# Optimization experiments

Measured on AMD Instinct MI355X. Metric: run time of the kernel, lower is better.

Reference implementation:

```python
import jax, jax.numpy as jnp
import numpy as np

B, S, T, C = 4, 2048, 2048, 256
TEMPERATURE = 0.1
CONF_THR = 0.2
NEG_INF = -jnp.inf


def setup_inputs() -> dict:
    key = jax.random.key(0)
    k1, k2, k3 = jax.random.split(key, 3)
    src_feats = jax.random.normal(k1, (B, S, C), dtype=jnp.float32)
    tgt_feats = jax.random.normal(k2, (B, T, C), dtype=jnp.float32)
    # variable valid lengths per batch (padding masks)
    src_lens = jnp.array([2048, 1800, 1500, 1024])
    tgt_lens = jnp.array([2048, 1600, 2000, 1200])
    src_mask = jnp.arange(S)[None, :] < src_lens[:, None]
    tgt_mask = jnp.arange(T)[None, :] < tgt_lens[:, None]
    W = jax.random.normal(k3, (C, C), dtype=jnp.float32) * (C ** -0.5)
    return {"src_feats": src_feats, "tgt_feats": tgt_feats,
            "src_mask": src_mask, "tgt_mask": tgt_mask, "W": W}


def reference(src_feats, tgt_feats, src_mask, tgt_mask, W):
    # NOTE: original module applies src_proj to BOTH src and tgt (tgt_proj unused)
    src = jnp.einsum('bsc,dc->bsd', src_feats, W)  # Linear, no bias
    tgt = jnp.einsum('btc,dc->btd', tgt_feats, W)
    scale = src.shape[-1] ** 0.5
    src = src / scale
    tgt = tgt / scale
    sim = jnp.einsum('bsc,btc->bst', src, tgt) / TEMPERATURE  # [B,S,T]
    sim1 = jnp.where(src_mask[:, :, None], sim, NEG_INF)
    sim2 = jnp.where(tgt_mask[:, None, :], sim, NEG_INF)
    conf_matrix = jax.nn.softmax(sim1, axis=1) * jax.nn.softmax(sim2, axis=2)
    # get_match (no_grad in original): mutual-max + threshold mask.
    # Returned as a dense boolean mask (jit-safe), instead of nonzero() indices.
    m = conf_matrix > CONF_THR
    m = m & (conf_matrix == jnp.max(conf_matrix, axis=2, keepdims=True)) \
          & (conf_matrix == jnp.max(conf_matrix, axis=1, keepdims=True))
    return conf_matrix, m
```

## Files before the change

### kernel.cpp

```cpp
#include <hip/hip_runtime.h>
#include <hip/hip_bf16.h>
#include <cstdint>
#include <cstddef>

#define B_ 4
#define S_ 2048
#define T_ 2048
#define C_ 256
#define K2_ 512
#define NEG_INF (-INFINITY)

typedef __attribute__((ext_vector_type(8)))  __bf16 bf16x8;
typedef __attribute__((ext_vector_type(16))) float  f32x16;

#define ROWPAT(r, lh) (((r) & 3) + 8 * ((r) >> 2) + 4 * (lh))

typedef __attribute__((address_space(3))) unsigned       as3_u32;
typedef __attribute__((address_space(1))) const unsigned as1_u32;

__device__ __forceinline__ void gload16(const void* g, void* l) {
    __builtin_amdgcn_global_load_lds((as1_u32*)g, (as3_u32*)l, 16, 0, 0);
}

__device__ __forceinline__ unsigned pack_hl(float v) {
    __bf16 h = (__bf16)v;
    __bf16 l = (__bf16)(v - (float)h);
    unsigned short hu = __builtin_bit_cast(unsigned short, h);
    unsigned short lu = __builtin_bit_cast(unsigned short, l);
    return (unsigned)hu | ((unsigned)lu << 16);
}

__global__ void build_masks_kernel(const void* __restrict__ src_mask,
                                   const void* __restrict__ tgt_mask,
                                   int* __restrict__ smask, int* __restrict__ tmask) {
    int i = blockIdx.x * blockDim.x + threadIdx.x;
    const unsigned char* sb = (const unsigned char*)src_mask;
    const unsigned char* tb = (const unsigned char*)tgt_mask;
    bool s_is_byte = (sb[1] != 0);
    bool t_is_byte = (tb[1] != 0);
    if (i < B_ * S_)
        smask[i] = s_is_byte ? (sb[i] != 0) : (((const int*)src_mask)[i] != 0);
    if (i < B_ * T_)
        tmask[i] = t_is_byte ? (tb[i] != 0) : (((const int*)tgt_mask)[i] != 0);
}

__global__ __launch_bounds__(256) void split_kernel(
    const float* __restrict__ in, unsigned* __restrict__ out, int n4)
{
    for (int i = blockIdx.x * blockDim.x + threadIdx.x; i < n4;
         i += gridDim.x * blockDim.x) {
        float4 x = ((const float4*)in)[i];
        uint4 o;
        o.x = pack_hl(x.x); o.y = pack_hl(x.y);
        o.z = pack_hl(x.z); o.w = pack_hl(x.w);
        ((uint4*)out)[i] = o;
    }
}

template <int MODE>
__global__ __launch_bounds__(512, 2) void simgemm_kernel(
    const __bf16* __restrict__ A2g, const __bf16* __restrict__ B2g,
    const int* __restrict__ smask, const int* __restrict__ tmask,
    float2* __restrict__ rowpart, float2* __restrict__ colpart,
    const float2* __restrict__ rowstats, const float2* __restrict__ colstats,
    float* __restrict__ conf, unsigned* __restrict__ rowconfmax,
    unsigned* __restrict__ colconfmax, unsigned* __restrict__ P2out)
{
    __shared__ char lds[2 * 65536 + 256 * 4 * 2 + 256 * 8 * 2];
    char* bufs = lds;
    int*    smask_lds = (int*)(lds + 131072);
    int*    tmask_lds = smask_lds + 256;
    float2* rstat_lds = (float2*)(tmask_lds + 256);
    float2* cstat_lds = rstat_lds + 256;

    const int tid = threadIdx.x;
    const int w = tid >> 6, lane = tid & 63;
    const int wr = w >> 2, wc = w & 3;
    const int lr = lane & 31, lh = lane >> 5;

    int b = 0, m0, n0;
    const __bf16 *Ab, *Bb;
    if (MODE == 2) {
        m0 = blockIdx.x * 256; n0 = 0;
        Ab = A2g; Bb = B2g;
    } else {
        int lin = (blockIdx.x & 7) * 32 + (blockIdx.x >> 3);
        b = lin >> 6;
        int r = lin & 63;
        m0 = (r >> 3) * 256;
        n0 = (r & 7) * 256;
        Ab = A2g + (size_t)b * S_ * K2_;
        Bb = B2g + (size_t)b * T_ * K2_;
        if (tid < 256) {
            smask_lds[tid] = smask[b * S_ + m0 + tid];
            if (MODE == 1) rstat_lds[tid] = rowstats[b * S_ + m0 + tid];
        } else {
            int t = tid - 256;
            tmask_lds[t] = tmask[b * T_ + n0 + t];
            if (MODE == 1) cstat_lds[t] = colstats[b * T_ + n0 + t];
        }
    }

    auto stage = [&](int st) {
        char* buf = bufs + (st & 1) * 65536;
        const int kb = st * 64;
        #pragma unroll
        for (int q = 0; q < 4; ++q) {
            int i = q * 512 + tid;
            int row = i >> 3, c = i & 7;
            int sc = c ^ (row & 7);
            gload16(Ab + (size_t)(m0 + row) * K2_ + kb + sc * 8,
                    buf + (q * 512 + w * 64) * 16);
        }
        char* bufB = buf + 32768;
        #pragma unroll
        for (int q = 0; q < 4; ++q) {
            int i = q * 512 + tid;
            int row = i >> 3, c = i & 7;
            int sc = c ^ (row & 7);
            gload16(Bb + (size_t)(n0 + row) * K2_ + kb + sc * 8,
                    bufB + (q * 512 + w * 64) * 16);
        }
    };

    f32x16 acc[4][2] = {};
    stage(0);
    __syncthreads();
    for (int st = 0; st < 8; ++st) {
        if (st < 7) stage(st + 1);
        const char* buf  = bufs + (st & 1) * 65536;
        const char* bufB = buf + 32768;
        #pragma unroll
        for (int ks = 0; ks < 4; ++ks) {
            const int cs = ks * 2 + lh;
            bf16x8 a[4], bv[2], bs[2];
            #pragma unroll
            for (int fi = 0; fi < 4; ++fi) {
                int row = wr * 128 + fi * 32 + lr;
                a[fi] = *(const bf16x8*)(buf + row * 128 + ((cs ^ (row & 7)) * 16));
            }
            #pragma unroll
            for (int fj = 0; fj < 2; ++fj) {
                int row = wc * 64 + fj * 32 + lr;
                bv[fj] = *(const bf16x8*)(bufB + row * 128 + ((cs ^ (row & 7)) * 16));
                bs[fj] = __builtin_shufflevector(bv[fj], bv[fj], 1, 0, 3, 2, 5, 4, 7, 6);
            }
            #pragma unroll
            for (int fi = 0; fi < 4; ++fi)
                #pragma unroll
                for (int fj = 0; fj < 2; ++fj)
                    acc[fi][fj] = __builtin_amdgcn_mfma_f32_32x32x16_bf16(
                        a[fi], bv[fj], acc[fi][fj], 0, 0, 0);
            #pragma unroll
            for (int fi = 0; fi < 4; ++fi)
                #pragma unroll
                for (int fj = 0; fj < 2; ++fj)
                    acc[fi][fj] = __builtin_amdgcn_mfma_f32_32x32x16_bf16(
                        a[fi], bs[fj], acc[fi][fj], 0, 0, 0);
        }
        __syncthreads();
    }

    if (MODE == 2) {
        #pragma unroll
        for (int fi = 0; fi < 4; ++fi)
            #pragma unroll
            for (int fj = 0; fj < 2; ++fj)
                #pragma unroll
                for (int r = 0; r < 16; ++r) {
                    int row = m0 + wr * 128 + fi * 32 + ROWPAT(r, lh);
                    int col = wc * 64 + fj * 32 + lr;
                    P2out[(size_t)row * 256 + col] = pack_hl(acc[fi][fj][r] * 0.0625f);
                }
        return;
    }

    if (MODE == 0) {
        const int tm0 = tmask_lds[wc * 64 + lr];
        const int tm1 = tmask_lds[wc * 64 + 32 + lr];
        #pragma unroll
        for (int fi = 0; fi < 4; ++fi)
            #pragma unroll
            for (int r = 0; r < 16; ++r) {
                float v0 = tm0 ? acc[fi][0][r] * 10.f : NEG_INF;
                float v1 = tm1 ? acc[fi][1][r] * 10.f : NEG_INF;
                float m = fmaxf(v0, v1);
                #pragma unroll
                for (int off = 1; off <= 16; off <<= 1)
                    m = fmaxf(m, __shfl_xor(m, off));
                float e = 0.f;
                if (m > NEG_INF) e = __expf(v0 - m) + __expf(v1 - m);
                #pragma unroll
                for (int off = 1; off <= 16; off <<= 1)
                    e += __shfl_xor(e, off);
                if (lr == 0) {
                    int row = m0 + wr * 128 + fi * 32 + ROWPAT(r, lh);
                    rowpart[((size_t)(b * S_ + row)) * 32 + (n0 >> 6) + wc] =
                        make_float2(m, e);
                }
            }
        #pragma unroll
        for (int fj = 0; fj < 2; ++fj) {
            float m = NEG_INF;
            #pragma unroll
            for (int fi = 0; fi < 4; ++fi)
                #pragma unroll
                for (int r = 0; r < 16; ++r) {
                    int rl = wr * 128 + fi * 32 + ROWPAT(r, lh);
                    float x = smask_lds[rl] ? acc[fi][fj][r] * 10.f : NEG_INF;
                    m = fmaxf(m, x);
                }
            m = fmaxf(m, __shfl_xor(m, 32));
            float e = 0.f;
            if (m > NEG_INF) {
                #pragma unroll
                for (int fi = 0; fi < 4; ++fi)
                    #pragma unroll
                    for (int r = 0; r < 16; ++r) {
                        int rl = wr * 128 + fi * 32 + ROWPAT(r, lh);
                        float x = smask_lds[rl] ? acc[fi][fj][r] * 10.f : NEG_INF;
                        e += __expf(x - m);
                    }
            }
            e += __shfl_xor(e, 32);
            if (lh == 0) {
                int col = n0 + wc * 64 + fj * 32 + lr;
                colpart[((size_t)(b * T_ + col)) * 16 + (m0 >> 7) + wr] =
                    make_float2(m, e);
            }
        }
        return;
    }

    {
        const int tm0 = tmask_lds[wc * 64 + lr];
        const int tm1 = tmask_lds[wc * 64 + 32 + lr];
        float2 c0 = cstat_lds[wc * 64 + lr];
        float2 c1 = cstat_lds[wc * 64 + 32 + lr];
        const float cm0 = c0.x, ic0 = 1.f / c0.y;
        const float cm1 = c1.x, ic1 = 1.f / c1.y;
        float* confb = conf + (size_t)b * S_ * T_;
        float cmax0 = 0.f, cmax1 = 0.f;
        #pragma unroll
        for (int fi = 0; fi < 4; ++fi)
            #pragma unroll
            for (int r = 0; r < 16; ++r) {
                int rl = wr * 128 + fi * 32 + ROWPAT(r, lh);
                float2 rst = rstat_lds[rl];
                int sm = smask_lds[rl];
                float rm = rst.x, ir = 1.f / rst.y;
                float x0 = acc[fi][0][r] * 10.f;
                float x1 = acc[fi][1][r] * 10.f;
                float cv0 = (sm && tm0)
                    ? __expf(2.f * x0 - cm0 - rm) * (ic0 * ir) : 0.f;
                float cv1 = (sm && tm1)
                    ? __expf(2.f * x1 - cm1 - rm) * (ic1 * ir) : 0.f;
                int rg = m0 + rl;
                int cg = n0 + wc * 64 + lr;
                confb[(size_t)rg * T_ + cg]      = cv0;
                confb[(size_t)rg * T_ + cg + 32] = cv1;
                float rmx = fmaxf(cv0, cv1);
                #pragma unroll
                for (int off = 1; off <= 16; off <<= 1)
                    rmx = fmaxf(rmx, __shfl_xor(rmx, off));
                if (lr == 0)
                    atomicMax(&rowconfmax[b * S_ + rg], __float_as_uint(rmx));
                cmax0 = fmaxf(cmax0, cv0);
                cmax1 = fmaxf(cmax1, cv1);
            }
        cmax0 = fmaxf(cmax0, __shfl_xor(cmax0, 32));
        cmax1 = fmaxf(cmax1, __shfl_xor(cmax1, 32));
        if (lh == 0) {
            int cg = n0 + wc * 64 + lr;
            atomicMax(&colconfmax[b * T_ + cg],      __float_as_uint(cmax0));
            atomicMax(&colconfmax[b * T_ + cg + 32], __float_as_uint(cmax1));
        }
    }
}

__global__ __launch_bounds__(256) void combine_kernel(
    const float2* __restrict__ part, float2* __restrict__ stats, int n, int width)
{
    int r = blockIdx.x * 256 + threadIdx.x;
    if (r >= n) return;
    const float2* p = part + (size_t)r * width;
    float M = NEG_INF;
    for (int q = 0; q < width; ++q) M = fmaxf(M, p[q].x);
    float SS = 0.f;
    if (M > NEG_INF)
        for (int q = 0; q < width; ++q) SS += p[q].y * __expf(p[q].x - M);
    stats[r] = make_float2(M, SS);
}

__global__ __launch_bounds__(256) void maskout_kernel(
    const float* __restrict__ conf,
    const unsigned* __restrict__ rowconfmax, const unsigned* __restrict__ colconfmax,
    float* __restrict__ outmask)
{
    const size_t n4 = (size_t)B_ * S_ * T_ / 4;
    for (size_t i4 = (size_t)blockIdx.x * blockDim.x + threadIdx.x; i4 < n4;
         i4 += (size_t)gridDim.x * blockDim.x) {
        size_t base = i4 * 4;
        int t0  = (int)(base & (T_ - 1));
        int row = (int)(base >> 11);
        int b   = row >> 11;
        float4 c = *(const float4*)(conf + base);
        float rm = __uint_as_float(rowconfmax[row]);
        const unsigned* cmp = colconfmax + b * T_ + t0;
        float cc[4] = {c.x, c.y, c.z, c.w};
        float o[4];
        #pragma unroll
        for (int j = 0; j < 4; ++j) {
            float cmv = __uint_as_float(cmp[j]);
            o[j] = (cc[j] > 0.2f && cc[j] == rm && cc[j] == cmv) ? 1.f : 0.f;
        }
        *(float4*)(outmask + base) = make_float4(o[0], o[1], o[2], o[3]);
    }
}

extern "C" void kernel_launch(void* const* d_in, const int* in_sizes, int n_in,
                              void* d_out, int out_size, void* d_ws, size_t ws_size,
                              hipStream_t stream)
{
    const float* src_feats = (const float*)d_in[0];
    const float* tgt_feats = (const float*)d_in[1];
    const void*  src_mask  = d_in[2];
    const void*  tgt_mask  = d_in[3];
    const float* W         = (const float*)d_in[4];

    float* conf    = (float*)d_out;
    char*  maskreg = (char*)d_out + (size_t)B_ * S_ * T_ * 4;

    const size_t MB = 1024 * 1024;
    unsigned* feats2u = (unsigned*)(maskreg);
    unsigned* P2u     = (unsigned*)(maskreg + 16 * MB);
    unsigned* W2u     = (unsigned*)(maskreg + 32 * MB);
    float2* rowpart   = (float2*)(maskreg + 33 * MB);
    float2* colpart   = (float2*)(maskreg + 35 * MB);

    const __bf16* feats2 = (const __bf16*)feats2u;
    const __bf16* W2     = (const __bf16*)W2u;
    const __bf16* P2src  = (const __bf16*)P2u;
    const __bf16* P2tgt  = P2src + (size_t)B_ * S_ * K2_;

    float2*   rowstats   = (float2*)d_ws;
    float2*   colstats   = rowstats + B_ * S_;
    unsigned* rowconfmax = (unsigned*)(colstats + B_ * T_);
    unsigned* colconfmax = rowconfmax + B_ * S_;
    int*      smask      = (int*)(colconfmax + B_ * T_);
    int*      tmask      = smask + B_ * S_;

    hipMemsetAsync(rowconfmax, 0, (size_t)(B_ * S_ + B_ * T_) * sizeof(unsigned),
                   stream);
    build_masks_kernel<<<(B_ * S_ + 255) / 256, 256, 0, stream>>>(
        src_mask, tgt_mask, smask, tmask);

    split_kernel<<<2048, 256, 0, stream>>>(src_feats, feats2u, B_ * S_ * C_ / 4);
    split_kernel<<<2048, 256, 0, stream>>>(
        tgt_feats, feats2u + (size_t)B_ * S_ * C_, B_ * T_ * C_ / 4);
    split_kernel<<<64, 256, 0, stream>>>(W, W2u, C_ * C_ / 4);

    simgemm_kernel<2><<<(2 * B_ * S_) / 256, 512, 0, stream>>>(
        feats2, W2, nullptr, nullptr, nullptr, nullptr, nullptr, nullptr,
        nullptr, nullptr, nullptr, P2u);

    simgemm_kernel<0><<<(S_ / 256) * (T_ / 256) * B_, 512, 0, stream>>>(
        P2src, P2tgt, smask, tmask, rowpart, colpart,
        nullptr, nullptr, nullptr, nullptr, nullptr, nullptr);

    combine_kernel<<<(B_ * S_ + 255) / 256, 256, 0, stream>>>(
        rowpart, rowstats, B_ * S_, 32);
    combine_kernel<<<(B_ * T_ + 255) / 256, 256, 0, stream>>>(
        colpart, colstats, B_ * T_, 16);

    simgemm_kernel<1><<<(S_ / 256) * (T_ / 256) * B_, 512, 0, stream>>>(
        P2src, P2tgt, smask, tmask, nullptr, nullptr,
        rowstats, colstats, conf, rowconfmax, colconfmax, nullptr);

    maskout_kernel<<<2048, 256, 0, stream>>>(conf, rowconfmax, colconfmax,
                                             (float*)maskreg);
}
```

Measured before the change: 304.0 us.

## Fuse all stages into one cooperative persistent kernel with grid syncs

Replaces the split, projection GEMM, two similarity GEMMs, combine and maskout launches with a single cooperative kernel using grid-wide syncs. Each block keeps its similarity tile in registers across phases, so the second similarity GEMM and the re-read of conf for mask generation are avoided. The projection is done in-kernel with on-the-fly fp32-to-bf16 hi/lo splitting. This trades launch and recompute cost for grid-sync overhead and a reliance on all 256 blocks being co-resident.

```diff
diff --git a/kernel.cpp b/kernel.cpp
--- a/kernel.cpp
+++ b/kernel.cpp
@@ -1,7 +1,10 @@
 #include <hip/hip_runtime.h>
 #include <hip/hip_bf16.h>
+#include <hip/hip_cooperative_groups.h>
 #include <cstdint>
 #include <cstddef>
+
+namespace cg = cooperative_groups;
 
 #define B_ 4
 #define S_ 2048
@@ -28,6 +31,13 @@
     unsigned short hu = __builtin_bit_cast(unsigned short, h);
     unsigned short lu = __builtin_bit_cast(unsigned short, l);
     return (unsigned)hu | ((unsigned)lu << 16);
+}
+
+__device__ __noinline__ float conf_fn(float a, float rm, float rs, float cm,
+                                      float cs, int on) {
+    float x = a * 10.f;
+    float v = __expf(2.f * x - cm - rm) / (rs * cs);
+    return on ? v : 0.f;
 }
 
 __global__ void build_masks_kernel(const void* __restrict__ src_mask,
@@ -44,29 +54,17 @@
         tmask[i] = t_is_byte ? (tb[i] != 0) : (((const int*)tgt_mask)[i] != 0);
 }
 
-__global__ __launch_bounds__(256) void split_kernel(
-    const float* __restrict__ in, unsigned* __restrict__ out, int n4)
+__global__ __launch_bounds__(512, 2) void fused_kernel(
+    const float* __restrict__ src_feats, const float* __restrict__ tgt_feats,
+    const float* __restrict__ Wf,
+    const int* __restrict__ smask, const int* __restrict__ tmask,
+    unsigned* __restrict__ P2u,
+    float2* __restrict__ rowpart, float2* __restrict__ colpart,
+    float2* __restrict__ rowstats, float2* __restrict__ colstats,
+    unsigned* __restrict__ rowconfmax, unsigned* __restrict__ colconfmax,
+    float* __restrict__ conf, float* __restrict__ maskoutp)
 {
-    for (int i = blockIdx.x * blockDim.x + threadIdx.x; i < n4;
-         i += gridDim.x * blockDim.x) {
-        float4 x = ((const float4*)in)[i];
-        uint4 o;
-        o.x = pack_hl(x.x); o.y = pack_hl(x.y);
-        o.z = pack_hl(x.z); o.w = pack_hl(x.w);
-        ((uint4*)out)[i] = o;
-    }
-}
-
-template <int MODE>
-__global__ __launch_bounds__(512, 2) void simgemm_kernel(
-    const __bf16* __restrict__ A2g, const __bf16* __restrict__ B2g,
-    const int* __restrict__ smask, const int* __restrict__ tmask,
-    float2* __restrict__ rowpart, float2* __restrict__ colpart,
-    const float2* __restrict__ rowstats, const float2* __restrict__ colstats,
-    float* __restrict__ conf, unsigned* __restrict__ rowconfmax,
-    unsigned* __restrict__ colconfmax, unsigned* __restrict__ P2out)
-{
-    __shared__ char lds[2 * 65536 + 256 * 4 * 2 + 256 * 8 * 2];
+    __shared__ char lds[131072 + 256 * 4 * 2 + 256 * 8 * 2];
     char* bufs = lds;
     int*    smask_lds = (int*)(lds + 131072);
     int*    tmask_lds = smask_lds + 256;
@@ -75,31 +73,86 @@
 
     const int tid = threadIdx.x;
     const int w = tid >> 6, lane = tid & 63;
+    const int lr = lane & 31, lh = lane >> 5;
+
+    const int lin = (blockIdx.x & 7) * 32 + (blockIdx.x >> 3);
+    const int b = lin >> 6;
+    const int rr = lin & 63;
+    const int m0 = (rr >> 3) * 256;
+    const int n0 = (rr & 7) * 256;
     const int wr = w >> 2, wc = w & 3;
-    const int lr = lane & 31, lh = lane >> 5;
-
-    int b = 0, m0, n0;
-    const __bf16 *Ab, *Bb;
-    if (MODE == 2) {
-        m0 = blockIdx.x * 256; n0 = 0;
-        Ab = A2g; Bb = B2g;
-    } else {
-        int lin = (blockIdx.x & 7) * 32 + (blockIdx.x >> 3);
-        b = lin >> 6;
-        int r = lin & 63;
-        m0 = (r >> 3) * 256;
-        n0 = (r & 7) * 256;
-        Ab = A2g + (size_t)b * S_ * K2_;
-        Bb = B2g + (size_t)b * T_ * K2_;
-        if (tid < 256) {
-            smask_lds[tid] = smask[b * S_ + m0 + tid];
-            if (MODE == 1) rstat_lds[tid] = rowstats[b * S_ + m0 + tid];
-        } else {
-            int t = tid - 256;
-            tmask_lds[t] = tmask[b * T_ + n0 + t];
-            if (MODE == 1) cstat_lds[t] = colstats[b * T_ + n0 + t];
-        }
-    }
+
+    if (tid < 256) smask_lds[tid] = smask[b * S_ + m0 + tid];
+    else           tmask_lds[tid - 256] = tmask[b * T_ + n0 + (tid - 256)];
+
+    {
+        char* pA = bufs;
+        char* pW = bufs + 8192;
+        const int m0p = blockIdx.x * 64;
+        const float* Fbase = (m0p < B_ * S_)
+            ? (src_feats + (size_t)m0p * C_)
+            : (tgt_feats + (size_t)(m0p - B_ * S_) * C_);
+        f32x16 acc0[2] = {};
+        for (int st = 0; st < 8; ++st) {
+            {
+                int row = tid >> 3, c8 = tid & 7;
+                float4 av = *(const float4*)(Fbase + (size_t)row * C_ +
+                                             st * 32 + c8 * 4);
+                uint4 p = make_uint4(pack_hl(av.x), pack_hl(av.y),
+                                     pack_hl(av.z), pack_hl(av.w));
+                *(uint4*)(pA + row * 128 + ((c8 ^ (row & 7)) * 16)) = p;
+            }
+            #pragma unroll
+            for (int q = 0; q < 4; ++q) {
+                int i = q * 512 + tid;
+                int row = i >> 3, c8 = i & 7;
+                float4 wv = *(const float4*)(Wf + (size_t)row * C_ +
+                                             st * 32 + c8 * 4);
+                uint4 p = make_uint4(pack_hl(wv.x), pack_hl(wv.y),
+                                     pack_hl(wv.z), pack_hl(wv.w));
+                *(uint4*)(pW + row * 128 + ((c8 ^ (row & 7)) * 16)) = p;
+            }
+            __syncthreads();
+            #pragma unroll
+            for (int ks = 0; ks < 4; ++ks) {
+                const int cs = ks * 2 + lh;
+                bf16x8 a0[2], bw, bs;
+                #pragma unroll
+                for (int fi = 0; fi < 2; ++fi) {
+                    int row = fi * 32 + lr;
+                    a0[fi] = *(const bf16x8*)(pA + row * 128 +
+                                              ((cs ^ (row & 7)) * 16));
+                }
+                {
+                    int row = w * 32 + lr;
+                    bw = *(const bf16x8*)(pW + row * 128 +
+                                          ((cs ^ (row & 7)) * 16));
+                    bs = __builtin_shufflevector(bw, bw, 1, 0, 3, 2, 5, 4, 7, 6);
+                }
+                #pragma unroll
+                for (int fi = 0; fi < 2; ++fi) {
+                    acc0[fi] = __builtin_amdgcn_mfma_f32_32x32x16_bf16(
+                        a0[fi], bw, acc0[fi], 0, 0, 0);
+                    acc0[fi] = __builtin_amdgcn_mfma_f32_32x32x16_bf16(
+                        a0[fi], bs, acc0[fi], 0, 0, 0);
+                }
+            }
+            __syncthreads();
+        }
+        #pragma unroll
+        for (int fi = 0; fi < 2; ++fi)
+            #pragma unroll
+            for (int r = 0; r < 16; ++r) {
+                int row = m0p + fi * 32 + ROWPAT(r, lh);
+                int col = w * 32 + lr;
+                P2u[(size_t)row * 256 + col] = pack_hl(acc0[fi][r] * 0.0625f);
+            }
+    }
+    cg::this_grid().sync();
+
+    const __bf16* P2 = (const __bf16*)P2u;
+    const __bf16* Ab = P2 + (size_t)(b * S_) * K2_;
+    const __bf16* Bb = P2 + (size_t)(B_ * S_ + b * T_) * K2_;
 
     auto stage = [&](int st) {
         char* buf = bufs + (st & 1) * 65536;
@@ -161,21 +214,7 @@
         __syncthreads();
     }
 
-    if (MODE == 2) {
-        #pragma unroll
-        for (int fi = 0; fi < 4; ++fi)
-            #pragma unroll
-            for (int fj = 0; fj < 2; ++fj)
-                #pragma unroll
-                for (int r = 0; r < 16; ++r) {
-                    int row = m0 + wr * 128 + fi * 32 + ROWPAT(r, lh);
-                    int col = wc * 64 + fj * 32 + lr;
-                    P2out[(size_t)row * 256 + col] = pack_hl(acc[fi][fj][r] * 0.0625f);
-                }
-        return;
-    }
-
-    if (MODE == 0) {
+    {
         const int tm0 = tmask_lds[wc * 64 + lr];
         const int tm1 = tmask_lds[wc * 64 + 32 + lr];
         #pragma unroll
@@ -229,16 +268,51 @@
                     make_float2(m, e);
             }
         }
-        return;
-    }
+    }
+    cg::this_grid().sync();
 
     {
-        const int tm0 = tmask_lds[wc * 64 + lr];
-        const int tm1 = tmask_lds[wc * 64 + 32 + lr];
-        float2 c0 = cstat_lds[wc * 64 + lr];
-        float2 c1 = cstat_lds[wc * 64 + 32 + lr];
-        const float cm0 = c0.x, ic0 = 1.f / c0.y;
-        const float cm1 = c1.x, ic1 = 1.f / c1.y;
+        const int bid = blockIdx.x;
+        #pragma unroll
+        for (int rq = 0; rq < 2; ++rq) {
+            int row = bid * 32 + (tid >> 5) * 2 + rq;
+            float2 p = rowpart[(size_t)row * 32 + (tid & 31)];
+            float M = p.x;
+            #pragma unroll
+            for (int off = 1; off <= 16; off <<= 1)
+                M = fmaxf(M, __shfl_xor(M, off));
+            float e = p.y * __expf(p.x - M);
+            #pragma unroll
+            for (int off = 1; off <= 16; off <<= 1)
+                e += __shfl_xor(e, off);
+            if ((tid & 31) == 0) rowstats[row] = make_float2(M, e);
+        }
+        {
+            int col = bid * 32 + (tid >> 4);
+            float2 p = colpart[(size_t)col * 16 + (tid & 15)];
+            float M = p.x;
+            #pragma unroll
+            for (int off = 1; off <= 8; off <<= 1)
+                M = fmaxf(M, __shfl_xor(M, off));
+            float e = p.y * __expf(p.x - M);
+            #pragma unroll
+            for (int off = 1; off <= 8; off <<= 1)
+                e += __shfl_xor(e, off);
+            if ((tid & 15) == 0) colstats[col] = make_float2(M, e);
+        }
+        if (tid < 32)            rowconfmax[bid * 32 + tid] = 0u;
+        else if (tid < 64)       colconfmax[bid * 32 + tid - 32] = 0u;
+    }
+    cg::this_grid().sync();
+
+    if (tid < 256) rstat_lds[tid] = rowstats[b * S_ + m0 + tid];
+    else           cstat_lds[tid - 256] = colstats[b * T_ + n0 + (tid - 256)];
+    __syncthreads();
+    const int tm0 = tmask_lds[wc * 64 + lr];
+    const int tm1 = tmask_lds[wc * 64 + 32 + lr];
+    const float2 cst0 = cstat_lds[wc * 64 + lr];
+    const float2 cst1 = cstat_lds[wc * 64 + 32 + lr];
+    {
         float* confb = conf + (size_t)b * S_ * T_;
         float cmax0 = 0.f, cmax1 = 0.f;
         #pragma unroll
@@ -248,13 +322,10 @@
                 int rl = wr * 128 + fi * 32 + ROWPAT(r, lh);
                 float2 rst = rstat_lds[rl];
                 int sm = smask_lds[rl];
-                float rm = rst.x, ir = 1.f / rst.y;
-                float x0 = acc[fi][0][r] * 10.f;
-                float x1 = acc[fi][1][r] * 10.f;
-                float cv0 = (sm && tm0)
-                    ? __expf(2.f * x0 - cm0 - rm) * (ic0 * ir) : 0.f;
-                float cv1 = (sm && tm1)
-                    ? __expf(2.f * x1 - cm1 - rm) * (ic1 * ir) : 0.f;
+                float cv0 = conf_fn(acc[fi][0][r], rst.x, rst.y, cst0.x, cst0.y,
+                                    sm && tm0);
+                float cv1 = conf_fn(acc[fi][1][r], rst.x, rst.y, cst1.x, cst1.y,
+                                    sm && tm1);
                 int rg = m0 + rl;
                 int cg = n0 + wc * 64 + lr;
                 confb[(size_t)rg * T_ + cg]      = cv0;
@@ -276,45 +347,31 @@
             atomicMax(&colconfmax[b * T_ + cg + 32], __float_as_uint(cmax1));
         }
     }
-}
-
-__global__ __launch_bounds__(256) void combine_kernel(
-    const float2* __restrict__ part, float2* __restrict__ stats, int n, int width)
-{
-    int r = blockIdx.x * 256 + threadIdx.x;
-    if (r >= n) return;
-    const float2* p = part + (size_t)r * width;
-    float M = NEG_INF;
-    for (int q = 0; q < width; ++q) M = fmaxf(M, p[q].x);
-    float SS = 0.f;
-    if (M > NEG_INF)
-        for (int q = 0; q < width; ++q) SS += p[q].y * __expf(p[q].x - M);
-    stats[r] = make_float2(M, SS);
-}
-
-__global__ __launch_bounds__(256) void maskout_kernel(
-    const float* __restrict__ conf,
-    const unsigned* __restrict__ rowconfmax, const unsigned* __restrict__ colconfmax,
-    float* __restrict__ outmask)
-{
-    const size_t n4 = (size_t)B_ * S_ * T_ / 4;
-    for (size_t i4 = (size_t)blockIdx.x * blockDim.x + threadIdx.x; i4 < n4;
-         i4 += (size_t)gridDim.x * blockDim.x) {
-        size_t base = i4 * 4;
-        int t0  = (int)(base & (T_ - 1));
-        int row = (int)(base >> 11);
-        int b   = row >> 11;
-        float4 c = *(const float4*)(conf + base);
-        float rm = __uint_as_float(rowconfmax[row]);
-        const unsigned* cmp = colconfmax + b * T_ + t0;
-        float cc[4] = {c.x, c.y, c.z, c.w};
-        float o[4];
-        #pragma unroll
-        for (int j = 0; j < 4; ++j) {
-            float cmv = __uint_as_float(cmp[j]);
-            o[j] = (cc[j] > 0.2f && cc[j] == rm && cc[j] == cmv) ? 1.f : 0.f;
-        }
-        *(float4*)(outmask + base) = make_float4(o[0], o[1], o[2], o[3]);
+    cg::this_grid().sync();
+
+    {
+        float* maskb = maskoutp + (size_t)b * S_ * T_;
+        const int cg = n0 + wc * 64 + lr;
+        const float cmax0f = __uint_as_float(colconfmax[b * T_ + cg]);
+        const float cmax1f = __uint_as_float(colconfmax[b * T_ + cg + 32]);
+        #pragma unroll
+        for (int fi = 0; fi < 4; ++fi)
+            #pragma unroll
+            for (int r = 0; r < 16; ++r) {
+                int rl = wr * 128 + fi * 32 + ROWPAT(r, lh);
+                float2 rst = rstat_lds[rl];
+                int sm = smask_lds[rl];
+                int rg = m0 + rl;
+                float rmaxf = __uint_as_float(rowconfmax[b * S_ + rg]);
+                float cv0 = conf_fn(acc[fi][0][r], rst.x, rst.y, cst0.x, cst0.y,
+                                    sm && tm0);
+                float cv1 = conf_fn(acc[fi][1][r], rst.x, rst.y, cst1.x, cst1.y,
+                                    sm && tm1);
+                float o0 = (cv0 > 0.2f && cv0 == rmaxf && cv0 == cmax0f) ? 1.f : 0.f;
+                float o1 = (cv1 > 0.2f && cv1 == rmaxf && cv1 == cmax1f) ? 1.f : 0.f;
+                maskb[(size_t)rg * T_ + cg]      = o0;
+                maskb[(size_t)rg * T_ + cg + 32] = o1;
+            }
     }
 }
 
@@ -326,22 +383,15 @@
     const float* tgt_feats = (const float*)d_in[1];
     const void*  src_mask  = d_in[2];
     const void*  tgt_mask  = d_in[3];
-    const float* W         = (const float*)d_in[4];
+    const float* Wf        = (const float*)d_in[4];
 
     float* conf    = (float*)d_out;
-    char*  maskreg = (char*)d_out + (size_t)B_ * S_ * T_ * 4;
+    float* maskreg = conf + (size_t)B_ * S_ * T_;
 
     const size_t MB = 1024 * 1024;
-    unsigned* feats2u = (unsigned*)(maskreg);
-    unsigned* P2u     = (unsigned*)(maskreg + 16 * MB);
-    unsigned* W2u     = (unsigned*)(maskreg + 32 * MB);
-    float2* rowpart   = (float2*)(maskreg + 33 * MB);
-    float2* colpart   = (float2*)(maskreg + 35 * MB);
-
-    const __bf16* feats2 = (const __bf16*)feats2u;
-    const __bf16* W2     = (const __bf16*)W2u;
-    const __bf16* P2src  = (const __bf16*)P2u;
-    const __bf16* P2tgt  = P2src + (size_t)B_ * S_ * K2_;
+    unsigned* P2u     = (unsigned*)maskreg;
+    float2*   rowpart = (float2*)((char*)maskreg + 16 * MB);
+    float2*   colpart = (float2*)((char*)maskreg + 18 * MB);
 
     float2*   rowstats   = (float2*)d_ws;
     float2*   colstats   = rowstats + B_ * S_;
@@ -350,33 +400,16 @@
     int*      smask      = (int*)(colconfmax + B_ * T_);
     int*      tmask      = smask + B_ * S_;
 
-    hipMemsetAsync(rowconfmax, 0, (size_t)(B_ * S_ + B_ * T_) * sizeof(unsigned),
-                   stream);
-    build_masks_kernel<<<(B_ * S_ + 255) / 256, 256, 0, stream>>>(
-        src_mask, tgt_mask, smask, tmask);
-
-    split_kernel<<<2048, 256, 0, stream>>>(src_feats, feats2u, B_ * S_ * C_ / 4);
-    split_kernel<<<2048, 256, 0, stream>>>(
-        tgt_feats, feats2u + (size_t)B_ * S_ * C_, B_ * T_ * C_ / 4);
-    split_kernel<<<64, 256, 0, stream>>>(W, W2u, C_ * C_ / 4);
-
-    simgemm_kernel<2><<<(2 * B_ * S_) / 256, 512, 0, stream>>>(
-        feats2, W2, nullptr, nullptr, nullptr, nullptr, nullptr, nullptr,
-        nullptr, nullptr, nullptr, P2u);
-
-    simgemm_kernel<0><<<(S_ / 256) * (T_ / 256) * B_, 512, 0, stream>>>(
-        P2src, P2tgt, smask, tmask, rowpart, colpart,
-        nullptr, nullptr, nullptr, nullptr, nullptr, nullptr);
-
-    combine_kernel<<<(B_ * S_ + 255) / 256, 256, 0, stream>>>(
-        rowpart, rowstats, B_ * S_, 32);
-    combine_kernel<<<(B_ * T_ + 255) / 256, 256, 0, stream>>>(
-        colpart, colstats, B_ * T_, 16);
-
-    simgemm_kernel<1><<<(S_ / 256) * (T_ / 256) * B_, 512, 0, stream>>>(
-        P2src, P2tgt, smask, tmask, nullptr, nullptr,
-        rowstats, colstats, conf, rowconfmax, colconfmax, nullptr);
-
-    maskout_kernel<<<2048, 256, 0, stream>>>(conf, rowconfmax, colconfmax,
-                                             (float*)maskreg);
-}
+    build_masks_kernel<<<32, 256, 0, stream>>>(src_mask, tgt_mask, smask, tmask);
+
+    void* args[] = {
+        (void*)&src_feats, (void*)&tgt_feats, (void*)&Wf,
+        (void*)&smask, (void*)&tmask, (void*)&P2u,
+        (void*)&rowpart, (void*)&colpart,
+        (void*)&rowstats, (void*)&colstats,
+        (void*)&rowconfmax, (void*)&colconfmax,
+        (void*)&conf, (void*)&maskreg
+    };
+    hipLaunchCooperativeKernel((const void*)fused_kernel, dim3(256), dim3(512),
+                               args, 0, stream);
+}
```

Result: slower. 437.7 us (+44.0%).
